# Kernel optimization log

Measured on AMD Instinct MI355X. Metric: run time of the kernel, lower is better.

Reference implementation:

```python
import jax, jax.numpy as jnp
import numpy as np

N = 100000; E = 1600000; D_IN = 128; HID = 64; HEADS = 2; OUT = 2; B = 8192
NEG_SLOPE = 0.2


def gat_conv(x, edge_index, W, a_src, a_dst, bias):
    """PyG-style GATConv with add_self_loops=True, concat=False (mean over heads).
    x: [N, Fin], W: [Fin, H*C], a_src/a_dst: [H, C], bias: [C]."""
    n = x.shape[0]
    H, C = a_src.shape
    h = (x @ W).reshape(n, H, C)                      # [N,H,C]
    s_src = (h * a_src[None]).sum(-1)                 # [N,H]
    s_dst = (h * a_dst[None]).sum(-1)                 # [N,H]
    loop = jnp.arange(n, dtype=edge_index.dtype)
    src = jnp.concatenate([edge_index[0], loop])      # [E+N]
    dst = jnp.concatenate([edge_index[1], loop])
    e = jax.nn.leaky_relu(s_src[src] + s_dst[dst], NEG_SLOPE)   # [E+N,H]
    # segment softmax over edges grouped by destination node
    m = jax.ops.segment_max(e, dst, num_segments=n)             # [N,H]
    ex = jnp.exp(e - m[dst])
    z = jax.ops.segment_sum(ex, dst, num_segments=n)            # [N,H]
    alpha = ex / z[dst]                                          # [E+N,H]
    msg = h[src] * alpha[:, :, None]                             # [E+N,H,C]
    out = jax.ops.segment_sum(msg, dst, num_segments=n)         # [N,H,C]
    return out.mean(axis=1) + bias                               # concat=False -> mean over heads


def setup_inputs() -> dict:
    key = jax.random.key(0)
    ks = jax.random.split(key, 32)
    def p(k, shape, fan_in):
        return (jax.random.normal(k, shape, dtype=jnp.float32) / np.sqrt(fan_in)).astype(jnp.float32)
    inp = {}
    inp["x_l"] = jax.random.normal(ks[0], (N, D_IN), dtype=jnp.float32)
    inp["x_r"] = jax.random.normal(ks[1], (N, D_IN), dtype=jnp.float32)
    inp["edge_index_l"] = jax.random.randint(ks[2], (2, E), 0, N, dtype=jnp.int64 if jax.config.jax_enable_x64 else jnp.int32)
    inp["edge_index_r"] = jax.random.randint(ks[3], (2, E), 0, N, dtype=jnp.int64 if jax.config.jax_enable_x64 else jnp.int32)
    inp["labels_l"] = jax.random.randint(ks[4], (B,), 0, N)
    inp["labels_r"] = jax.random.randint(ks[5], (B,), 0, N)
    i = 6
    for side in ("l", "r"):
        inp[f"w1{side}"] = p(ks[i], (D_IN, HEADS * HID), D_IN); i += 1
        inp[f"as1{side}"] = p(ks[i], (HEADS, HID), HID); i += 1
        inp[f"ad1{side}"] = p(ks[i], (HEADS, HID), HID); i += 1
        inp[f"b1{side}"] = jnp.zeros((HID,), jnp.float32)
        inp[f"w2{side}"] = p(ks[i], (HID, HEADS * HID), HID); i += 1
        inp[f"as2{side}"] = p(ks[i], (HEADS, HID), HID); i += 1
        inp[f"ad2{side}"] = p(ks[i], (HEADS, HID), HID); i += 1
        inp[f"b2{side}"] = jnp.zeros((HID,), jnp.float32)
    inp["fc1_w"] = p(ks[i], (2 * HID, HID), 2 * HID); i += 1
    inp["fc1_b"] = jnp.zeros((HID,), jnp.float32)
    inp["fc2_w"] = p(ks[i], (HID, OUT), HID); i += 1
    inp["fc2_b"] = jnp.zeros((OUT,), jnp.float32)
    return inp


def reference(x_l, x_r, edge_index_l, edge_index_r, labels_l, labels_r,
              w1l, as1l, ad1l, b1l, w2l, as2l, ad2l, b2l,
              w1r, as1r, ad1r, b1r, w2r, as2r, ad2r, b2r,
              fc1_w, fc1_b, fc2_w, fc2_b):
    # left tower (dropout is identity in eval mode)
    hl = jax.nn.relu(gat_conv(x_l, edge_index_l, w1l, as1l, ad1l, b1l))
    hl = jax.nn.relu(gat_conv(hl, edge_index_l, w2l, as2l, ad2l, b2l))
    # right tower
    hr = jax.nn.relu(gat_conv(x_r, edge_index_r, w1r, as1r, ad1r, b1r))
    hr = jax.nn.relu(gat_conv(hr, edge_index_r, w2r, as2r, ad2r, b2r))
    # merge_graphs: gather node features per labeled pair, concat
    merged = jnp.concatenate([hl[labels_l], hr[labels_r]], axis=-1)  # [B, 2*HID]
    x = jax.nn.relu(merged @ fc1_w + fc1_b)
    return x @ fc2_w + fc2_b
```

## Files before the change

### kernel.cpp

```cpp
#include <hip/hip_runtime.h>
#include <hip/hip_bf16.h>
#include <hip/hip_fp16.h>

constexpr int NN   = 100000;
constexpr int EE   = 1600000;
constexpr int BB   = 8192;
constexpr int PAD  = 48;
constexpr float NEG_SLOPE = 0.2f;

constexpr int GBM = 128, GBK = 16;
constexpr int XSTR = GBM + 4;
constexpr int GB = (NN + GBM - 1) / GBM;
constexpr int AB2 = NN / 8;

constexpr int BSPAN = 256;
constexpr int NB    = (NN + BSPAN - 1) / BSPAN;
constexpr int BCAP  = 5120;
constexpr int CHA   = 4096;
constexpr int NCH   = (EE + CHA - 1) / CHA;

__device__ __forceinline__ float4 ld4(const float* p) { return *(const float4*)p; }
__device__ __forceinline__ float4 ld4(const __half* p) {
    __half2 a = *(const __half2*)p;
    __half2 b = *(const __half2*)(p + 2);
    float2 fa = __half22float2(a), fb = __half22float2(b);
    return make_float4(fa.x, fa.y, fb.x, fb.y);
}

template <typename TIN>
__device__ __forceinline__
void gemm_body(int bid, const TIN* __restrict__ x, int K,
               const float* __restrict__ W,
               const float* __restrict__ a_src, const float* __restrict__ a_dst,
               __half* __restrict__ h,
               float* __restrict__ ssrc, float* __restrict__ sdst,
               float* xs, float* ws) {
    const int tx = threadIdx.x & 15;
    const int ty = threadIdx.x >> 4;
    const int row0 = bid * GBM;
    const int col0 = tx * 8;

    const int c0 = (2 * tx)     ^ (((2 * tx)     & 8) >> 3);
    const int c1 = (2 * tx + 1) ^ (((2 * tx + 1) & 8) >> 3);

    float acc[8][8];
    #pragma unroll
    for (int i = 0; i < 8; ++i)
        #pragma unroll
        for (int j = 0; j < 8; ++j) acc[i][j] = 0.f;

    for (int kt = 0; kt < K; kt += GBK) {
        __syncthreads();
        #pragma unroll
        for (int i = 0; i < 2; ++i) {
            int idx = threadIdx.x + i * 256;
            int row = idx >> 2, cc = idx & 3;
            int grow = row0 + row; if (grow >= NN) grow = NN - 1;
            const float4 v = ld4(&x[(size_t)grow * K + kt + cc * 4]);
            int kb = cc * 4;
            xs[(kb + 0) * XSTR + row] = v.x;
            xs[(kb + 1) * XSTR + row] = v.y;
            xs[(kb + 2) * XSTR + row] = v.z;
            xs[(kb + 3) * XSTR + row] = v.w;
        }
        #pragma unroll
        for (int i = 0; i < 2; ++i) {
            int idx = threadIdx.x + i * 256;
            int kk = idx >> 5, c = idx & 31;
            int cs = c ^ ((c & 8) >> 3);
            *(float4*)&ws[kk * 128 + cs * 4] =
                *(const float4*)&W[(size_t)(kt + kk) * 128 + c * 4];
        }
        __syncthreads();

        #pragma unroll
        for (int kk = 0; kk < GBK; ++kk) {
            float4 a0 = *(const float4*)&xs[kk * XSTR + ty * 8];
            float4 a1 = *(const float4*)&xs[kk * XSTR + ty * 8 + 4];
            float4 b0 = *(const float4*)&ws[kk * 128 + c0 * 4];
            float4 b1 = *(const float4*)&ws[kk * 128 + c1 * 4];
            float av[8] = {a0.x, a0.y, a0.z, a0.w, a1.x, a1.y, a1.z, a1.w};
            float bv[8] = {b0.x, b0.y, b0.z, b0.w, b1.x, b1.y, b1.z, b1.w};
            #pragma unroll
            for (int i = 0; i < 8; ++i)
                #pragma unroll
                for (int j = 0; j < 8; ++j)
                    acc[i][j] = fmaf(av[i], bv[j], acc[i][j]);
        }
    }

    float asv[8], adv[8];
    #pragma unroll
    for (int j = 0; j < 8; ++j) { asv[j] = a_src[col0 + j]; adv[j] = a_dst[col0 + j]; }
    const int head = tx >> 3;

    #pragma unroll
    for (int i = 0; i < 8; ++i) {
        int row = row0 + ty * 8 + i;
        bool ok = row < NN;
        if (ok) {
            __align__(16) __half2 hp[4];
            hp[0] = __floats2half2_rn(acc[i][0], acc[i][1]);
            hp[1] = __floats2half2_rn(acc[i][2], acc[i][3]);
            hp[2] = __floats2half2_rn(acc[i][4], acc[i][5]);
            hp[3] = __floats2half2_rn(acc[i][6], acc[i][7]);
            *(int4*)&h[(size_t)row * 128 + col0] = *(int4*)hp;
        }
        float ps = 0.f, pd = 0.f;
        #pragma unroll
        for (int j = 0; j < 8; ++j) {
            ps = fmaf(acc[i][j], asv[j], ps);
            pd = fmaf(acc[i][j], adv[j], pd);
        }
        ps += __shfl_xor(ps, 1); pd += __shfl_xor(pd, 1);
        ps += __shfl_xor(ps, 2); pd += __shfl_xor(pd, 2);
        ps += __shfl_xor(ps, 4); pd += __shfl_xor(pd, 4);
        if (ok && (tx & 7) == 0) {
            ssrc[row * 2 + head] = ps;
            sdst[row * 2 + head] = pd;
        }
    }
}

__global__ __launch_bounds__(256)
void k_bucket(const int* __restrict__ el, const int* __restrict__ er,
              int2* __restrict__ buf, int* __restrict__ gcur) {
    __shared__ int2 P0[CHA];
    __shared__ int2 P1[CHA];
    __shared__ int hist[NB];
    __shared__ int st[NB];
    __shared__ int ofs[NB];
    __shared__ int base[NB];
    __shared__ int sc[512];

    const int blk = blockIdx.x;
    const bool right = blk >= NCH;
    const int* __restrict__ e = right ? er : el;
    const int sideoff = right ? NB : 0;
    const int cbase = (right ? blk - NCH : blk) * CHA;
    int cnum = EE - cbase; if (cnum > CHA) cnum = CHA;
    const int t = threadIdx.x;

    for (int i = t; i < cnum; i += 256) {
        int2 p; p.x = e[EE + cbase + i]; p.y = e[cbase + i];
        P0[i] = p;
    }
    for (int i = t; i < NB; i += 256) hist[i] = 0;
    __syncthreads();
    for (int i = t; i < cnum; i += 256) atomicAdd(&hist[P0[i].x >> 8], 1);
    __syncthreads();

    sc[t]       = (t < NB)       ? hist[t]       : 0;
    sc[t + 256] = (t + 256 < NB) ? hist[t + 256] : 0;
    __syncthreads();
    for (int off = 1; off < 512; off <<= 1) {
        int a0 = sc[t];
        int a1 = sc[t + 256];
        int b0 = (t >= off)       ? sc[t - off]       : 0;
        int b1 = (t + 256 >= off) ? sc[t + 256 - off] : 0;
        __syncthreads();
        sc[t] = a0 + b0;
        sc[t + 256] = a1 + b1;
        __syncthreads();
    }
    for (int i = t; i < NB; i += 256) {
        int s = sc[i] - hist[i];
        st[i] = s;
        ofs[i] = s;
    }
    __syncthreads();
    for (int i = t; i < cnum; i += 256) {
        int2 p = P0[i];
        int pos = atomicAdd(&ofs[p.x >> 8], 1);
        P1[pos] = p;
    }
    __syncthreads();
    for (int i = t; i < NB; i += 256)
        base[i] = hist[i] ? atomicAdd(&gcur[sideoff + i], hist[i]) : 0;
    __syncthreads();
    for (int j = t; j < cnum; j += 256) {
        int2 p = P1[j];
        int bk = p.x >> 8;
        buf[(size_t)(sideoff + bk) * BCAP + base[bk] + (j - st[bk])] = p;
    }
}

__global__ __launch_bounds__(256)
void k_csr(const int2* __restrict__ buf, const int* __restrict__ gcur,
           int* __restrict__ cntl, int* __restrict__ cntr,
           int* __restrict__ csrl, int* __restrict__ csrr) {
    __shared__ int lcnt[BSPAN];
    __shared__ __align__(16) int lcsr[BSPAN * PAD];

    const int blk = blockIdx.x;
    const bool right = blk >= NB;
    const int bk = right ? blk - NB : blk;
    int* __restrict__ cnt = right ? cntr : cntl;
    int* __restrict__ csr = right ? csrr : csrl;
    const int2* __restrict__ src = buf + (size_t)blk * BCAP;
    const int count = gcur[blk];
    const int lo = bk * BSPAN;
    int nn = NN - lo; if (nn > BSPAN) nn = BSPAN;
    const int t = threadIdx.x;

    for (int i = t; i < nn; i += 256) lcnt[i] = 0;
    __syncthreads();
    for (int i = t; i < count; i += 256) {
        int2 p = src[i];
        int ld = p.x - lo;
        int slot = atomicAdd(&lcnt[ld], 1);
        lcsr[ld * PAD + slot] = p.y;
    }
    __syncthreads();
    const int tot4 = (nn * PAD) >> 2;
    int4* __restrict__ dst4 = (int4*)&csr[(size_t)lo * PAD];
    const int4* __restrict__ s4 = (const int4*)lcsr;
    for (int i = t; i < tot4; i += 256) dst4[i] = s4[i];
    for (int i = t; i < nn; i += 256) cnt[lo + i] = lcnt[i];
}

__global__ __launch_bounds__(256)
void k_gemm1(const float* __restrict__ x_l, const float* __restrict__ x_r,
             const float* __restrict__ w1l, const float* __restrict__ as1l,
             const float* __restrict__ ad1l,
             const float* __restrict__ w1r, const float* __restrict__ as1r,
             const float* __restrict__ ad1r,
             __half* __restrict__ h_l, __half* __restrict__ h_r,
             float* __restrict__ ssrc_l, float* __restrict__ sdst_l,
             float* __restrict__ ssrc_r, float* __restrict__ sdst_r) {
    __shared__ float smem[GBK * XSTR + GBK * 128];
    int b = blockIdx.x;
    if (b < GB)
        gemm_body<float>(b, x_l, 128, w1l, as1l, ad1l,
                         h_l, ssrc_l, sdst_l, smem, smem + GBK * XSTR);
    else
        gemm_body<float>(b - GB, x_r, 128, w1r, as1r, ad1r,
                         h_r, ssrc_r, sdst_r, smem, smem + GBK * XSTR);
}

__global__ __launch_bounds__(256)
void k_gemm2x(const __half* __restrict__ f_l, const __half* __restrict__ f_r,
              const float* __restrict__ w2l, const float* __restrict__ as2l,
              const float* __restrict__ ad2l,
              const float* __restrict__ w2r, const float* __restrict__ as2r,
              const float* __restrict__ ad2r,
              __half* __restrict__ h_l, __half* __restrict__ h_r,
              float* __restrict__ ssrc_l, float* __restrict__ sdst_l,
              float* __restrict__ ssrc_r, float* __restrict__ sdst_r) {
    __shared__ float smem[GBK * XSTR + GBK * 128];
    int b = blockIdx.x;
    if (b < GB)
        gemm_body<__half>(b, f_l, 64, w2l, as2l, ad2l,
                          h_l, ssrc_l, sdst_l, smem, smem + GBK * XSTR);
    else
        gemm_body<__half>(b - GB, f_r, 64, w2r, as2r, ad2r,
                          h_r, ssrc_r, sdst_r, smem, smem + GBK * XSTR);
}

__device__ __forceinline__
void att_body(int n, const __half* __restrict__ h,
              const float* __restrict__ ssrc, const float* __restrict__ sdst,
              const int* __restrict__ cnt, const int* __restrict__ csr,
              const float* __restrict__ bias, __half* __restrict__ out) {
    const int g  = threadIdx.x & 31;
    const int hs = g >> 4;
    const int j  = g & 15;
    const int ch = g * 4;

    float sd = sdst[n * 2 + hs];
    float es = ssrc[n * 2 + hs] + sd;
    es = es > 0.f ? es : NEG_SLOPE * es;
    const float wself = __expf(es);
    float zl = 0.f;

    uint2 sv = *(const uint2*)&h[(size_t)n * 128 + ch];
    __half2 sh0 = *(__half2*)&sv.x, sh1 = *(__half2*)&sv.y;
    float2 p01 = __half22float2(sh0), p23 = __half22float2(sh1);
    float a0 = wself * p01.x, a1 = wself * p01.y;
    float a2 = wself * p23.x, a3 = wself * p23.y;

    int b = n * PAD;
    const int e = b + cnt[n];
    while (b < e) {
        int c = e - b; if (c > 16) c = 16;
        int idx = b + (j < c ? j : c - 1);
        int sj = csr[idx];
        float ev = ssrc[sj * 2 + hs] + sd;
        ev = ev > 0.f ? ev : NEG_SLOPE * ev;
        float w = (j < c) ? __expf(ev) : 0.f;
        zl += w;
        int jj = 0;
        for (; jj + 4 <= c; jj += 4) {
            int s0 = __shfl(sj, jj,     32);
            int s1 = __shfl(sj, jj + 1, 32);
            int s2 = __shfl(sj, jj + 2, 32);
            int s3 = __shfl(sj, jj + 3, 32);
            float w0 = __shfl(w, hs * 16 + jj,     32);
            float w1 = __shfl(w, hs * 16 + jj + 1, 32);
            float w2 = __shfl(w, hs * 16 + jj + 2, 32);
            float w3 = __shfl(w, hs * 16 + jj + 3, 32);
            uint2 u0 = *(const uint2*)&h[(size_t)(unsigned)(s0 * 128 + ch)];
            uint2 u1 = *(const uint2*)&h[(size_t)(unsigned)(s1 * 128 + ch)];
            uint2 u2 = *(const uint2*)&h[(size_t)(unsigned)(s2 * 128 + ch)];
            uint2 u3 = *(const uint2*)&h[(size_t)(unsigned)(s3 * 128 + ch)];
            float2 f0a = __half22float2(*(__half2*)&u0.x), f0b = __half22float2(*(__half2*)&u0.y);
            float2 f1a = __half22float2(*(__half2*)&u1.x), f1b = __half22float2(*(__half2*)&u1.y);
            float2 f2a = __half22float2(*(__half2*)&u2.x), f2b = __half22float2(*(__half2*)&u2.y);
            float2 f3a = __half22float2(*(__half2*)&u3.x), f3b = __half22float2(*(__half2*)&u3.y);
            a0 = fmaf(w0, f0a.x, a0); a1 = fmaf(w0, f0a.y, a1);
            a2 = fmaf(w0, f0b.x, a2); a3 = fmaf(w0, f0b.y, a3);
            a0 = fmaf(w1, f1a.x, a0); a1 = fmaf(w1, f1a.y, a1);
            a2 = fmaf(w1, f1b.x, a2); a3 = fmaf(w1, f1b.y, a3);
            a0 = fmaf(w2, f2a.x, a0); a1 = fmaf(w2, f2a.y, a1);
            a2 = fmaf(w2, f2b.x, a2); a3 = fmaf(w2, f2b.y, a3);
            a0 = fmaf(w3, f3a.x, a0); a1 = fmaf(w3, f3a.y, a1);
            a2 = fmaf(w3, f3b.x, a2); a3 = fmaf(w3, f3b.y, a3);
        }
        for (; jj < c; ++jj) {
            int s0   = __shfl(sj, jj, 32);
            float w0 = __shfl(w, hs * 16 + jj, 32);
            uint2 u0 = *(const uint2*)&h[(size_t)(unsigned)(s0 * 128 + ch)];
            float2 f0a = __half22float2(*(__half2*)&u0.x), f0b = __half22float2(*(__half2*)&u0.y);
            a0 = fmaf(w0, f0a.x, a0); a1 = fmaf(w0, f0a.y, a1);
            a2 = fmaf(w0, f0b.x, a2); a3 = fmaf(w0, f0b.y, a3);
        }
        b += c;
    }

    zl += __shfl_xor(zl, 1, 32);
    zl += __shfl_xor(zl, 2, 32);
    zl += __shfl_xor(zl, 4, 32);
    zl += __shfl_xor(zl, 8, 32);
    const float z = wself + zl;

    float zi = 1.f / z;
    a0 *= zi; a1 *= zi; a2 *= zi; a3 *= zi;
    a0 = 0.5f * (a0 + __shfl_xor(a0, 16));
    a1 = 0.5f * (a1 + __shfl_xor(a1, 16));
    a2 = 0.5f * (a2 + __shfl_xor(a2, 16));
    a3 = 0.5f * (a3 + __shfl_xor(a3, 16));
    if (hs == 0) {
        float4 bv = *(const float4*)&bias[ch];
        a0 += bv.x; a1 += bv.y; a2 += bv.z; a3 += bv.w;
        a0 = a0 > 0.f ? a0 : 0.f;
        a1 = a1 > 0.f ? a1 : 0.f;
        a2 = a2 > 0.f ? a2 : 0.f;
        a3 = a3 > 0.f ? a3 : 0.f;
        __align__(8) __half2 hp[2];
        hp[0] = __floats2half2_rn(a0, a1);
        hp[1] = __floats2half2_rn(a2, a3);
        *(uint2*)&out[(size_t)n * 64 + ch] = *(uint2*)hp;
    }
}

__global__ __launch_bounds__(256)
void k_att2x(const __half* __restrict__ h_l, const __half* __restrict__ h_r,
             const float* __restrict__ ssrc_l, const float* __restrict__ sdst_l,
             const float* __restrict__ ssrc_r, const float* __restrict__ sdst_r,
             const int* __restrict__ cnt_l, const int* __restrict__ csr_l,
             const int* __restrict__ cnt_r, const int* __restrict__ csr_r,
             const float* __restrict__ bias_l, const float* __restrict__ bias_r,
             __half* __restrict__ feat_l, __half* __restrict__ feat_r) {
    int blk = blockIdx.x;
    bool right = blk >= AB2;
    int n = (blk - (right ? AB2 : 0)) * 8 + (threadIdx.x >> 5);
    if (!right) att_body(n, h_l, ssrc_l, sdst_l, cnt_l, csr_l, bias_l, feat_l);
    else        att_body(n, h_r, ssrc_r, sdst_r, cnt_r, csr_r, bias_r, feat_r);
}

__global__ __launch_bounds__(256)
void k_fc(const __half* __restrict__ fl, const __half* __restrict__ fr,
          const int* __restrict__ ll, const int* __restrict__ lr,
          const float* __restrict__ w1, const float* __restrict__ b1,
          const float* __restrict__ w2, const float* __restrict__ b2,
          float* __restrict__ out) {
    int b = blockIdx.x * 4 + (threadIdx.x >> 6);
    int j = threadIdx.x & 63;
    int la = ll[b], lb = lr[b];
    float v0 = __half2float(fl[(size_t)la * 64 + j]);
    float v1 = __half2float(fr[(size_t)lb * 64 + j]);
    float acc = b1[j];
    #pragma unroll 8
    for (int k = 0; k < 64; ++k)
        acc += __shfl(v0, k, 64) * w1[k * 64 + j];
    #pragma unroll 8
    for (int k = 0; k < 64; ++k)
        acc += __shfl(v1, k, 64) * w1[(64 + k) * 64 + j];
    float x1 = acc > 0.f ? acc : 0.f;
    float p0 = x1 * w2[j * 2 + 0];
    float p1 = x1 * w2[j * 2 + 1];
    #pragma unroll
    for (int o = 32; o >= 1; o >>= 1) {
        p0 += __shfl_xor(p0, o, 64);
        p1 += __shfl_xor(p1, o, 64);
    }
    if (j == 0) {
        out[b * 2 + 0] = p0 + b2[0];
        out[b * 2 + 1] = p1 + b2[1];
    }
}

extern "C" void kernel_launch(void* const* d_in, const int* in_sizes, int n_in,
                              void* d_out, int out_size, void* d_ws, size_t ws_size,
                              hipStream_t stream) {
    const float* x_l  = (const float*)d_in[0];
    const float* x_r  = (const float*)d_in[1];
    const int* ei_l  = (const int*)d_in[2];
    const int* ei_r  = (const int*)d_in[3];
    const int* lab_l = (const int*)d_in[4];
    const int* lab_r = (const int*)d_in[5];
    const float* w1l  = (const float*)d_in[6];
    const float* as1l = (const float*)d_in[7];
    const float* ad1l = (const float*)d_in[8];
    const float* b1l  = (const float*)d_in[9];
    const float* w2l  = (const float*)d_in[10];
    const float* as2l = (const float*)d_in[11];
    const float* ad2l = (const float*)d_in[12];
    const float* b2l  = (const float*)d_in[13];
    const float* w1r  = (const float*)d_in[14];
    const float* as1r = (const float*)d_in[15];
    const float* ad1r = (const float*)d_in[16];
    const float* b1r  = (const float*)d_in[17];
    const float* w2r  = (const float*)d_in[18];
    const float* as2r = (const float*)d_in[19];
    const float* ad2r = (const float*)d_in[20];
    const float* b2r  = (const float*)d_in[21];
    const float* fc1w = (const float*)d_in[22];
    const float* fc1b = (const float*)d_in[23];
    const float* fc2w = (const float*)d_in[24];
    const float* fc2b = (const float*)d_in[25];

    char* p = (char*)d_ws;
    auto alloc = [&](size_t bytes) -> void* {
        void* q = (void*)p;
        p += (bytes + 255) & ~(size_t)255;
        return q;
    };
    __half* h_l    = (__half*)alloc((size_t)NN * 128 * 2);
    __half* h_r    = (__half*)alloc((size_t)NN * 128 * 2);
    __half* feat_l = (__half*)alloc((size_t)NN * 64 * 2);
    __half* feat_r = (__half*)alloc((size_t)NN * 64 * 2);
    float* ssrc_l = (float*)alloc((size_t)NN * 2 * 4);
    float* sdst_l = (float*)alloc((size_t)NN * 2 * 4);
    float* ssrc_r = (float*)alloc((size_t)NN * 2 * 4);
    float* sdst_r = (float*)alloc((size_t)NN * 2 * 4);
    int* cnt2  = (int*)alloc(((size_t)2 * NN + 2 * NB) * 4);
    int* csr_l = (int*)alloc((size_t)NN * PAD * 4);
    int* csr_r = (int*)alloc((size_t)NN * PAD * 4);
    int* cnt_l = cnt2;
    int* cnt_r = cnt2 + NN;
    int* gcur  = cnt2 + 2 * NN;

    int2* buf = (int2*)h_l;

    hipMemsetAsync(gcur, 0, (size_t)2 * NB * 4, stream);

    k_bucket<<<2 * NCH, 256, 0, stream>>>(ei_l, ei_r, buf, gcur);

    k_csr<<<2 * NB, 256, 0, stream>>>(buf, gcur, cnt_l, cnt_r, csr_l, csr_r);

    k_gemm1<<<2 * GB, 256, 0, stream>>>(x_l, x_r,
                                        w1l, as1l, ad1l, w1r, as1r, ad1r,
                                        h_l, h_r, ssrc_l, sdst_l, ssrc_r, sdst_r);

    k_att2x<<<2 * AB2, 256, 0, stream>>>(h_l, h_r, ssrc_l, sdst_l, ssrc_r, sdst_r,
                                         cnt_l, csr_l, cnt_r, csr_r,
                                         b1l, b1r, feat_l, feat_r);

    k_gemm2x<<<2 * GB, 256, 0, stream>>>(feat_l, feat_r,
                                         w2l, as2l, ad2l, w2r, as2r, ad2r,
                                         h_l, h_r, ssrc_l, sdst_l, ssrc_r, sdst_r);

    k_att2x<<<2 * AB2, 256, 0, stream>>>(h_l, h_r, ssrc_l, sdst_l, ssrc_r, sdst_r,
                                         cnt_l, csr_l, cnt_r, csr_r,
                                         b2l, b2r, feat_l, feat_r);

    k_fc<<<(BB + 3) / 4, 256, 0, stream>>>(feat_l, feat_r, lab_l, lab_r,
                                           fc1w, fc1b, fc2w, fc2b,
                                           (float*)d_out);
}
```

Baseline: 617.1 us.

## Replace FP32 SIMT GEMMs with split-FP16 MFMA matrix-core kernels

Replaces the scalar FMA GEMM for both GAT layers with a templated kernel built on 16x16x32 f16 MFMA instructions. Inputs and weights are split into hi/lo half-precision parts and three MFMA passes are combined to keep close to FP32 accuracy. LDS tiles use an XOR-swizzled layout. This trades extra conversion work, the extra MFMA passes and larger shared memory (up to 64KB, which limits occupancy) for matrix-core throughput. Output h stores are now scalar half writes rather than vector writes.

```diff
diff --git a/kernel.cpp b/kernel.cpp
--- a/kernel.cpp
+++ b/kernel.cpp
@@ -8,8 +8,7 @@
 constexpr int PAD  = 48;
 constexpr float NEG_SLOPE = 0.2f;
 
-constexpr int GBM = 128, GBK = 16;
-constexpr int XSTR = GBM + 4;
+constexpr int GBM = 128;
 constexpr int GB = (NN + GBM - 1) / GBM;
 constexpr int AB2 = NN / 8;
 
@@ -19,105 +18,168 @@
 constexpr int CHA   = 4096;
 constexpr int NCH   = (EE + CHA - 1) / CHA;
 
+typedef _Float16 f16x8 __attribute__((ext_vector_type(8)));
+typedef _Float16 f16x4 __attribute__((ext_vector_type(4)));
+typedef float    f32x4 __attribute__((ext_vector_type(4)));
+
 __device__ __forceinline__ float4 ld4(const float* p) { return *(const float4*)p; }
-__device__ __forceinline__ float4 ld4(const __half* p) {
-    __half2 a = *(const __half2*)p;
-    __half2 b = *(const __half2*)(p + 2);
-    float2 fa = __half22float2(a), fb = __half22float2(b);
-    return make_float4(fa.x, fa.y, fb.x, fb.y);
-}
-
-template <typename TIN>
-__device__ __forceinline__
-void gemm_body(int bid, const TIN* __restrict__ x, int K,
-               const float* __restrict__ W,
-               const float* __restrict__ a_src, const float* __restrict__ a_dst,
-               __half* __restrict__ h,
-               float* __restrict__ ssrc, float* __restrict__ sdst,
-               float* xs, float* ws) {
-    const int tx = threadIdx.x & 15;
-    const int ty = threadIdx.x >> 4;
+
+template <typename TIN, int K>
+__global__ __launch_bounds__(256)
+void gemm_mfma(const TIN* __restrict__ xA, const TIN* __restrict__ xB,
+               const float* __restrict__ WA, const float* __restrict__ asA,
+               const float* __restrict__ adA,
+               const float* __restrict__ WB, const float* __restrict__ asB,
+               const float* __restrict__ adB,
+               __half* __restrict__ hA, __half* __restrict__ hB,
+               float* __restrict__ ssA, float* __restrict__ sdA,
+               float* __restrict__ ssB, float* __restrict__ sdB) {
+    constexpr bool HAS_LO = sizeof(TIN) == 4;
+    constexpr int LSZ = HAS_LO ? 65536 : 49152;
+    __shared__ __align__(16) char lds[LSZ];
+    char* const xh = lds;
+    char* const xl = HAS_LO ? (lds + 16384) : lds;
+    char* const wh = lds + (HAS_LO ? 32768 : 16384);
+    char* const wl = wh + 16384;
+
+    const int bid0 = blockIdx.x;
+    const bool right = bid0 >= GB;
+    const int bid = right ? bid0 - GB : bid0;
+    const TIN* __restrict__ x = right ? xB : xA;
+    const float* __restrict__ W = right ? WB : WA;
+    const float* __restrict__ a_src = right ? asB : asA;
+    const float* __restrict__ a_dst = right ? adB : adA;
+    __half* __restrict__ h = right ? hB : hA;
+    float* __restrict__ ssrc = right ? ssB : ssA;
+    float* __restrict__ sdst = right ? sdB : sdA;
+
+    const int tid = threadIdx.x;
+    const int wid = tid >> 6;
+    const int lane = tid & 63;
+    const int l15 = lane & 15;
+    const int lg = lane >> 4;
     const int row0 = bid * GBM;
-    const int col0 = tx * 8;
-
-    const int c0 = (2 * tx)     ^ (((2 * tx)     & 8) >> 3);
-    const int c1 = (2 * tx + 1) ^ (((2 * tx + 1) & 8) >> 3);
-
-    float acc[8][8];
+
+    f32x4 acc[2][8];
     #pragma unroll
-    for (int i = 0; i < 8; ++i)
+    for (int i = 0; i < 2; ++i)
         #pragma unroll
-        for (int j = 0; j < 8; ++j) acc[i][j] = 0.f;
-
-    for (int kt = 0; kt < K; kt += GBK) {
+        for (int j = 0; j < 8; ++j) acc[i][j] = (f32x4)0.f;
+
+    for (int kt = 0; kt < K; kt += 64) {
         __syncthreads();
-        #pragma unroll
-        for (int i = 0; i < 2; ++i) {
-            int idx = threadIdx.x + i * 256;
-            int row = idx >> 2, cc = idx & 3;
-            int grow = row0 + row; if (grow >= NN) grow = NN - 1;
-            const float4 v = ld4(&x[(size_t)grow * K + kt + cc * 4]);
-            int kb = cc * 4;
-            xs[(kb + 0) * XSTR + row] = v.x;
-            xs[(kb + 1) * XSTR + row] = v.y;
-            xs[(kb + 2) * XSTR + row] = v.z;
-            xs[(kb + 3) * XSTR + row] = v.w;
+        if constexpr (HAS_LO) {
+            #pragma unroll
+            for (int i = 0; i < 8; ++i) {
+                int idx = tid + i * 256;
+                int row = idx >> 4, c4 = idx & 15;
+                int grow = row0 + row; if (grow >= NN) grow = NN - 1;
+                float4 v = ld4(&x[(size_t)grow * K + kt + c4 * 4]);
+                f16x4 hv, lv;
+                float f0 = v.x; _Float16 h0 = (_Float16)f0; hv[0] = h0; lv[0] = (_Float16)(f0 - (float)h0);
+                float f1 = v.y; _Float16 h1 = (_Float16)f1; hv[1] = h1; lv[1] = (_Float16)(f1 - (float)h1);
+                float f2 = v.z; _Float16 h2 = (_Float16)f2; hv[2] = h2; lv[2] = (_Float16)(f2 - (float)h2);
+                float f3 = v.w; _Float16 h3 = (_Float16)f3; hv[3] = h3; lv[3] = (_Float16)(f3 - (float)h3);
+                int byt = row * 128 + ((c4 * 8) ^ ((row & 7) << 4));
+                *(f16x4*)(xh + byt) = hv;
+                *(f16x4*)(xl + byt) = lv;
+            }
+        } else {
+            #pragma unroll
+            for (int i = 0; i < 4; ++i) {
+                int idx = tid + i * 256;
+                int row = idx >> 3, c8 = idx & 7;
+                int grow = row0 + row; if (grow >= NN) grow = NN - 1;
+                uint4 v = *(const uint4*)&x[(size_t)grow * 64 + c8 * 8];
+                int byt = row * 128 + ((c8 * 16) ^ ((row & 7) << 4));
+                *(uint4*)(xh + byt) = v;
+            }
         }
         #pragma unroll
-        for (int i = 0; i < 2; ++i) {
-            int idx = threadIdx.x + i * 256;
-            int kk = idx >> 5, c = idx & 31;
-            int cs = c ^ ((c & 8) >> 3);
-            *(float4*)&ws[kk * 128 + cs * 4] =
-                *(const float4*)&W[(size_t)(kt + kk) * 128 + c * 4];
+        for (int i = 0; i < 8; ++i) {
+            int idx = tid + i * 256;
+            int kk = idx >> 5, c4 = idx & 31;
+            float4 v = ld4(&W[(size_t)(kt + kk) * 128 + c4 * 4]);
+            float f[4] = {v.x, v.y, v.z, v.w};
+            #pragma unroll
+            for (int j = 0; j < 4; ++j) {
+                int col = c4 * 4 + j;
+                _Float16 hi = (_Float16)f[j];
+                _Float16 lo = (_Float16)(f[j] - (float)hi);
+                int byt = col * 128 + ((kk * 2) ^ ((col & 7) << 4));
+                *(_Float16*)(wh + byt) = hi;
+                *(_Float16*)(wl + byt) = lo;
+            }
         }
         __syncthreads();
 
         #pragma unroll
-        for (int kk = 0; kk < GBK; ++kk) {
-            float4 a0 = *(const float4*)&xs[kk * XSTR + ty * 8];
-            float4 a1 = *(const float4*)&xs[kk * XSTR + ty * 8 + 4];
-            float4 b0 = *(const float4*)&ws[kk * 128 + c0 * 4];
-            float4 b1 = *(const float4*)&ws[kk * 128 + c1 * 4];
-            float av[8] = {a0.x, a0.y, a0.z, a0.w, a1.x, a1.y, a1.z, a1.w};
-            float bv[8] = {b0.x, b0.y, b0.z, b0.w, b1.x, b1.y, b1.z, b1.w};
+        for (int ks = 0; ks < 2; ++ks) {
+            const int koff = ks * 64 + lg * 16;
+            f16x8 ah[2], al[2];
             #pragma unroll
-            for (int i = 0; i < 8; ++i)
+            for (int rt = 0; rt < 2; ++rt) {
+                int row = wid * 32 + rt * 16 + l15;
+                int byt = row * 128 + (koff ^ ((row & 7) << 4));
+                ah[rt] = *(const f16x8*)(xh + byt);
+                if constexpr (HAS_LO) al[rt] = *(const f16x8*)(xl + byt);
+            }
+            #pragma unroll
+            for (int ct = 0; ct < 8; ++ct) {
+                int col = ct * 16 + l15;
+                int byt = col * 128 + (koff ^ ((col & 7) << 4));
+                f16x8 bh = *(const f16x8*)(wh + byt);
+                f16x8 bl = *(const f16x8*)(wl + byt);
                 #pragma unroll
-                for (int j = 0; j < 8; ++j)
-                    acc[i][j] = fmaf(av[i], bv[j], acc[i][j]);
+                for (int rt = 0; rt < 2; ++rt) {
+                    acc[rt][ct] = __builtin_amdgcn_mfma_f32_16x16x32_f16(ah[rt], bh, acc[rt][ct], 0, 0, 0);
+                    acc[rt][ct] = __builtin_amdgcn_mfma_f32_16x16x32_f16(ah[rt], bl, acc[rt][ct], 0, 0, 0);
+                    if constexpr (HAS_LO)
+                        acc[rt][ct] = __builtin_amdgcn_mfma_f32_16x16x32_f16(al[rt], bh, acc[rt][ct], 0, 0, 0);
+                }
+            }
         }
     }
 
-    float asv[8], adv[8];
+    float sv[8], dv[8];
     #pragma unroll
-    for (int j = 0; j < 8; ++j) { asv[j] = a_src[col0 + j]; adv[j] = a_dst[col0 + j]; }
-    const int head = tx >> 3;
-
+    for (int ct = 0; ct < 8; ++ct) {
+        sv[ct] = a_src[ct * 16 + l15];
+        dv[ct] = a_dst[ct * 16 + l15];
+    }
     #pragma unroll
-    for (int i = 0; i < 8; ++i) {
-        int row = row0 + ty * 8 + i;
-        bool ok = row < NN;
-        if (ok) {
-            __align__(16) __half2 hp[4];
-            hp[0] = __floats2half2_rn(acc[i][0], acc[i][1]);
-            hp[1] = __floats2half2_rn(acc[i][2], acc[i][3]);
-            hp[2] = __floats2half2_rn(acc[i][4], acc[i][5]);
-            hp[3] = __floats2half2_rn(acc[i][6], acc[i][7]);
-            *(int4*)&h[(size_t)row * 128 + col0] = *(int4*)hp;
-        }
-        float ps = 0.f, pd = 0.f;
+    for (int rt = 0; rt < 2; ++rt) {
         #pragma unroll
-        for (int j = 0; j < 8; ++j) {
-            ps = fmaf(acc[i][j], asv[j], ps);
-            pd = fmaf(acc[i][j], adv[j], pd);
-        }
-        ps += __shfl_xor(ps, 1); pd += __shfl_xor(pd, 1);
-        ps += __shfl_xor(ps, 2); pd += __shfl_xor(pd, 2);
-        ps += __shfl_xor(ps, 4); pd += __shfl_xor(pd, 4);
-        if (ok && (tx & 7) == 0) {
-            ssrc[row * 2 + head] = ps;
-            sdst[row * 2 + head] = pd;
+        for (int r = 0; r < 4; ++r) {
+            int row = row0 + wid * 32 + rt * 16 + lg * 4 + r;
+            bool ok = row < NN;
+            if (ok) {
+                #pragma unroll
+                for (int ct = 0; ct < 8; ++ct)
+                    h[(size_t)row * 128 + ct * 16 + l15] = __float2half(acc[rt][ct][r]);
+            }
+            float ps0 = 0.f, pd0 = 0.f, ps1 = 0.f, pd1 = 0.f;
+            #pragma unroll
+            for (int ct = 0; ct < 4; ++ct) {
+                ps0 = fmaf(acc[rt][ct][r], sv[ct], ps0);
+                pd0 = fmaf(acc[rt][ct][r], dv[ct], pd0);
+                ps1 = fmaf(acc[rt][ct + 4][r], sv[ct + 4], ps1);
+                pd1 = fmaf(acc[rt][ct + 4][r], dv[ct + 4], pd1);
+            }
+            ps0 += __shfl_xor(ps0, 1); pd0 += __shfl_xor(pd0, 1);
+            ps1 += __shfl_xor(ps1, 1); pd1 += __shfl_xor(pd1, 1);
+            ps0 += __shfl_xor(ps0, 2); pd0 += __shfl_xor(pd0, 2);
+            ps1 += __shfl_xor(ps1, 2); pd1 += __shfl_xor(pd1, 2);
+            ps0 += __shfl_xor(ps0, 4); pd0 += __shfl_xor(pd0, 4);
+            ps1 += __shfl_xor(ps1, 4); pd1 += __shfl_xor(pd1, 4);
+            ps0 += __shfl_xor(ps0, 8); pd0 += __shfl_xor(pd0, 8);
+            ps1 += __shfl_xor(ps1, 8); pd1 += __shfl_xor(pd1, 8);
+            if (ok && l15 == 0) {
+                ssrc[row * 2 + 0] = ps0;
+                ssrc[row * 2 + 1] = ps1;
+                sdst[row * 2 + 0] = pd0;
+                sdst[row * 2 + 1] = pd1;
+            }
         }
     }
 }
@@ -217,44 +279,6 @@
     const int4* __restrict__ s4 = (const int4*)lcsr;
     for (int i = t; i < tot4; i += 256) dst4[i] = s4[i];
     for (int i = t; i < nn; i += 256) cnt[lo + i] = lcnt[i];
-}
-
-__global__ __launch_bounds__(256)
-void k_gemm1(const float* __restrict__ x_l, const float* __restrict__ x_r,
-             const float* __restrict__ w1l, const float* __restrict__ as1l,
-             const float* __restrict__ ad1l,
-             const float* __restrict__ w1r, const float* __restrict__ as1r,
-             const float* __restrict__ ad1r,
-             __half* __restrict__ h_l, __half* __restrict__ h_r,
-             float* __restrict__ ssrc_l, float* __restrict__ sdst_l,
-             float* __restrict__ ssrc_r, float* __restrict__ sdst_r) {
-    __shared__ float smem[GBK * XSTR + GBK * 128];
-    int b = blockIdx.x;
-    if (b < GB)
-        gemm_body<float>(b, x_l, 128, w1l, as1l, ad1l,
-                         h_l, ssrc_l, sdst_l, smem, smem + GBK * XSTR);
-    else
-        gemm_body<float>(b - GB, x_r, 128, w1r, as1r, ad1r,
-                         h_r, ssrc_r, sdst_r, smem, smem + GBK * XSTR);
-}
-
-__global__ __launch_bounds__(256)
-void k_gemm2x(const __half* __restrict__ f_l, const __half* __restrict__ f_r,
-              const float* __restrict__ w2l, const float* __restrict__ as2l,
-              const float* __restrict__ ad2l,
-              const float* __restrict__ w2r, const float* __restrict__ as2r,
-              const float* __restrict__ ad2r,
-              __half* __restrict__ h_l, __half* __restrict__ h_r,
-              float* __restrict__ ssrc_l, float* __restrict__ sdst_l,
-              float* __restrict__ ssrc_r, float* __restrict__ sdst_r) {
-    __shared__ float smem[GBK * XSTR + GBK * 128];
-    int b = blockIdx.x;
-    if (b < GB)
-        gemm_body<__half>(b, f_l, 64, w2l, as2l, ad2l,
-                          h_l, ssrc_l, sdst_l, smem, smem + GBK * XSTR);
-    else
-        gemm_body<__half>(b - GB, f_r, 64, w2r, as2r, ad2r,
-                          h_r, ssrc_r, sdst_r, smem, smem + GBK * XSTR);
 }
 
 __device__ __forceinline__
@@ -459,17 +483,17 @@
 
     k_csr<<<2 * NB, 256, 0, stream>>>(buf, gcur, cnt_l, cnt_r, csr_l, csr_r);
 
-    k_gemm1<<<2 * GB, 256, 0, stream>>>(x_l, x_r,
-                                        w1l, as1l, ad1l, w1r, as1r, ad1r,
-                                        h_l, h_r, ssrc_l, sdst_l, ssrc_r, sdst_r);
+    gemm_mfma<float, 128><<<2 * GB, 256, 0, stream>>>(
+        x_l, x_r, w1l, as1l, ad1l, w1r, as1r, ad1r,
+        h_l, h_r, ssrc_l, sdst_l, ssrc_r, sdst_r);
 
     k_att2x<<<2 * AB2, 256, 0, stream>>>(h_l, h_r, ssrc_l, sdst_l, ssrc_r, sdst_r,
                                          cnt_l, csr_l, cnt_r, csr_r,
                                          b1l, b1r, feat_l, feat_r);
 
-    k_gemm2x<<<2 * GB, 256, 0, stream>>>(feat_l, feat_r,
-                                         w2l, as2l, ad2l, w2r, as2r, ad2r,
-                                         h_l, h_r, ssrc_l, sdst_l, ssrc_r, sdst_r);
+    gemm_mfma<__half, 64><<<2 * GB, 256, 0, stream>>>(
+        feat_l, feat_r, w2l, as2l, ad2l, w2r, as2r, ad2r,
+        h_l, h_r, ssrc_l, sdst_l, ssrc_r, sdst_r);
 
     k_att2x<<<2 * AB2, 256, 0, stream>>>(h_l, h_r, ssrc_l, sdst_l, ssrc_r, sdst_r,
                                          cnt_l, csr_l, cnt_r, csr_r,
```

After: 633.9 us. +2.7%, slower.
